# Optimization experiments

Hardware: AMD Instinct MI355X
Metric: run time of the kernel (lower is better)

## Reference

```python
import jax, jax.numpy as jnp
import numpy as np
import math

N_COARSE, N_FINE = 8192, 32768
DEC_DIM, ENC_DIM, OUT_DIM, K = 256, 128, 128, 16
LN_EPS = 1e-5


def setup_inputs() -> dict:
    key = jax.random.key(0)
    ks = jax.random.split(key, 16)
    s = lambda fan_in: 1.0 / math.sqrt(fan_in)
    return {
        "decoder_features": jax.random.normal(ks[0], (N_COARSE, DEC_DIM), jnp.float32),
        "decoder_pos": jax.random.normal(ks[1], (N_COARSE, 3), jnp.float32),
        "encoder_features": jax.random.normal(ks[2], (N_FINE, ENC_DIM), jnp.float32),
        "encoder_pos": jax.random.normal(ks[3], (N_FINE, 3), jnp.float32),
        "encoder_labels": jax.random.randint(ks[4], (N_FINE,), 0, 13, jnp.int64),
        # params (torch nn.Linear default init scale)
        "Wq": jax.random.uniform(ks[5], (DEC_DIM, ENC_DIM), jnp.float32, -s(ENC_DIM), s(ENC_DIM)),
        "bq": jnp.zeros((DEC_DIM,), jnp.float32),
        "Wk": jax.random.uniform(ks[6], (DEC_DIM, DEC_DIM), jnp.float32, -s(DEC_DIM), s(DEC_DIM)),
        "bk": jnp.zeros((DEC_DIM,), jnp.float32),
        "Wv": jax.random.uniform(ks[7], (DEC_DIM, DEC_DIM), jnp.float32, -s(DEC_DIM), s(DEC_DIM)),
        "bv": jnp.zeros((DEC_DIM,), jnp.float32),
        "W1": jax.random.uniform(ks[8], (OUT_DIM, DEC_DIM + ENC_DIM), jnp.float32, -s(DEC_DIM + ENC_DIM), s(DEC_DIM + ENC_DIM)),
        "b1": jnp.zeros((OUT_DIM,), jnp.float32),
        "W2": jax.random.uniform(ks[9], (OUT_DIM, OUT_DIM), jnp.float32, -s(OUT_DIM), s(OUT_DIM)),
        "b2": jnp.zeros((OUT_DIM,), jnp.float32),
        "ln_g": jnp.ones((OUT_DIM,), jnp.float32),
        "ln_b": jnp.zeros((OUT_DIM,), jnp.float32),
    }


def _knn_indices(encoder_pos, decoder_pos, k):
    # For each fine (encoder) point, k nearest coarse (decoder) points.
    # squared distances [N_fine, N_coarse]
    d2 = (
        jnp.sum(encoder_pos * encoder_pos, axis=1, keepdims=True)
        - 2.0 * encoder_pos @ decoder_pos.T
        + jnp.sum(decoder_pos * decoder_pos, axis=1)[None, :]
    )
    _, idx = jax.lax.top_k(-d2, k)  # [N_fine, K]
    return idx


def reference(decoder_features, decoder_pos, encoder_features, encoder_pos,
              encoder_labels, Wq, bq, Wk, bk, Wv, bv, W1, b1, W2, b2, ln_g, ln_b):
    idx = _knn_indices(encoder_pos, decoder_pos, K)            # [Nf, K]
    nbr = decoder_features[idx]                                 # [Nf, K, Dd]
    query = encoder_features @ Wq.T + bq                        # [Nf, Dd]
    keys = nbr @ Wk.T + bk                                      # [Nf, K, Dd]
    values = nbr @ Wv.T + bv                                    # [Nf, K, Dd]
    scores = jnp.einsum('nd,nkd->nk', query, keys) / math.sqrt(DEC_DIM)
    # segment softmax over edges grouped by fine target == softmax over K
    weights = jax.nn.softmax(scores, axis=-1)                   # [Nf, K]
    agg = jnp.einsum('nk,nkd->nd', weights, values)             # [Nf, Dd]
    combined = jnp.concatenate([agg, encoder_features], axis=-1)
    h = jax.nn.relu(combined @ W1.T + b1)
    up = h @ W2.T + b2                                          # [Nf, out]
    mu = jnp.mean(up, axis=-1, keepdims=True)
    var = jnp.var(up, axis=-1, keepdims=True)
    out = (up - mu) * jax.lax.rsqrt(var + LN_EPS) * ln_g + ln_b
    # dropout is identity in eval mode
    return (out, encoder_pos, encoder_labels)
```

## Files before the change

kernel.cpp:

```cpp
#include <hip/hip_runtime.h>
#include <hip/hip_bf16.h>

typedef __hip_bfloat16 bf16;
typedef unsigned short u16;

#define NC 8192
#define NF 32768
#define KNN 16
#define FMAXV 3.402823466e+38f

__device__ __forceinline__ float bfbits2f(u16 u){
  union { unsigned u; float f; } x; x.u = ((unsigned)u) << 16; return x.f;
}

__global__ __launch_bounds__(256) void k_prep(const float* __restrict__ dpos,
                                              const float* __restrict__ W1,
                                              const float* __restrict__ W2,
                                              float4* __restrict__ pos4,
                                              float4* __restrict__ W1eSa,
                                              float4* __restrict__ W1eSb,
                                              float4* __restrict__ W2Sa,
                                              float4* __restrict__ W2Sb){
  int g = blockIdx.x * 256 + threadIdx.x;
  if (g < 8192){
    float x = dpos[g * 3 + 0], y = dpos[g * 3 + 1], z = dpos[g * 3 + 2];
    float dd = __fadd_rn(__fadd_rn(__fmul_rn(x,x), __fmul_rn(y,y)), __fmul_rn(z,z));
    pos4[g] = make_float4(x, y, z, dd * 0.5f);
  } else if (g < 10240){
    int f = g - 8192; int c4 = f >> 6, jg = f & 63;
    W1eSa[f] = ((const float4*)(W1 + (size_t)(2 * jg) * 384 + 256))[c4];
  } else if (g < 12288){
    int f = g - 10240; int c4 = f >> 6, jg = f & 63;
    W1eSb[f] = ((const float4*)(W1 + (size_t)(2 * jg + 1) * 384 + 256))[c4];
  } else if (g < 14336){
    int f = g - 12288; int c4 = f >> 6, jg = f & 63;
    W2Sa[f] = ((const float4*)(W2 + (size_t)(2 * jg) * 128))[c4];
  } else if (g < 16384){
    int f = g - 14336; int c4 = f >> 6, jg = f & 63;
    W2Sb[f] = ((const float4*)(W2 + (size_t)(2 * jg + 1) * 128))[c4];
  }
}

__global__ __launch_bounds__(256) void k_wprod(const float* __restrict__ Wk,
                                               const float* __restrict__ Wv,
                                               const float* __restrict__ Wq,
                                               const float* __restrict__ W1,
                                               const float* __restrict__ bk,
                                               const float* __restrict__ bv,
                                               const float* __restrict__ bq,
                                               float* __restrict__ WkqS,
                                               float* __restrict__ WvuS,
                                               float* __restrict__ bkq,
                                               float* __restrict__ bvu,
                                               float* __restrict__ wbq,
                                               float* __restrict__ sbq){
  __shared__ float red[256];
  int b = blockIdx.x, t = threadIdx.x;
  if (b < 128){
    int c = b;
    float acc = 0.f;
    for (int j = 0; j < 256; ++j)
      acc = fmaf(Wk[(size_t)j * 256 + t], Wq[(size_t)j * 128 + c], acc);
    WkqS[(size_t)((t >> 2) * 128 + c) * 4 + (t & 3)] = acc;
    red[t] = bk[t] * Wq[(size_t)t * 128 + c];
    __syncthreads();
    for (int s = 128; s > 0; s >>= 1){ if (t < s) red[t] += red[t + s]; __syncthreads(); }
    if (t == 0) bkq[c] = red[0];
  } else if (b < 256){
    int h = b - 128;
    float acc = 0.f;
    for (int c2 = 0; c2 < 256; ++c2)
      acc = fmaf(Wv[(size_t)c2 * 256 + t], W1[(size_t)h * 384 + c2], acc);
    WvuS[(size_t)((t >> 2) * 128 + h) * 4 + (t & 3)] = acc;
    red[t] = bv[t] * W1[(size_t)h * 384 + t];
    __syncthreads();
    for (int s = 128; s > 0; s >>= 1){ if (t < s) red[t] += red[t + s]; __syncthreads(); }
    if (t == 0) bvu[h] = red[0];
  } else {
    float acc = 0.f;
    for (int j = 0; j < 256; ++j)
      acc = fmaf(Wk[(size_t)j * 256 + t], bq[j], acc);
    wbq[t] = acc;
    red[t] = bk[t] * bq[t];
    __syncthreads();
    for (int s = 128; s > 0; s >>= 1){ if (t < s) red[t] += red[t + s]; __syncthreads(); }
    if (t == 0) sbq[0] = red[0];
  }
}

__global__ __launch_bounds__(256) void k_dec(const float* __restrict__ df,
                                             const float4* __restrict__ WkqS,
                                             const float4* __restrict__ WvuS,
                                             const float* __restrict__ bkq,
                                             const float* __restrict__ bvu,
                                             const float* __restrict__ wbq,
                                             const float* __restrict__ sbq,
                                             bf16* __restrict__ Zd, bf16* __restrict__ Ud,
                                             float* __restrict__ bqK){
  __shared__ float part[16][16];
  int t = threadIdx.x;
  int g0 = blockIdx.x * 16;
  int half = __builtin_amdgcn_readfirstlane(t >> 7);
  int c = t & 127;
  const float4* W = half ? WvuS : WkqS;
  float acc[16];
  #pragma unroll
  for (int p = 0; p < 16; ++p) acc[p] = 0.f;
  for (int j4 = 0; j4 < 64; ++j4){
    float4 w = W[j4 * 128 + c];
    #pragma unroll
    for (int p = 0; p < 16; ++p){
      float4 a = ((const float4*)(df + (size_t)(g0 + p) * 256))[j4];
      acc[p] += w.x*a.x + w.y*a.y + w.z*a.z + w.w*a.w;
    }
  }
  float bias = half ? bvu[c] : bkq[c];
  bf16* dst = half ? Ud : Zd;
  #pragma unroll
  for (int p = 0; p < 16; ++p)
    dst[(size_t)(g0 + p) * 128 + c] = __float2bfloat16(acc[p] + bias);
  {
    int r = t >> 4, seg = t & 15;
    float s = 0.f;
    const float* dr = df + (size_t)(g0 + r) * 256 + seg * 16;
    const float* wq = wbq + seg * 16;
    #pragma unroll
    for (int e = 0; e < 16; ++e) s = fmaf(dr[e], wq[e], s);
    part[r][seg] = s;
  }
  __syncthreads();
  if (t < 16){
    float s = sbq[0];
    #pragma unroll
    for (int seg = 0; seg < 16; ++seg) s += part[t][seg];
    bqK[g0 + t] = s;
  }
}

__global__ __launch_bounds__(256) void k_attn(const float* __restrict__ epos,
                                              const float4* __restrict__ pos4,
                                              const float* __restrict__ ef,
                                              const bf16* __restrict__ Zd,
                                              const bf16* __restrict__ Ud,
                                              const float* __restrict__ bqK,
                                              bf16* __restrict__ hagg){
  __shared__ float smin[8 * 64];
  __shared__ float tauLDS[8];
  __shared__ int   cnt[8];
  __shared__ float lval[8][64];
  __shared__ int   lidx[8][64];

  int t = threadIdx.x, lane = t & 63, w = t >> 6;
  int n0 = blockIdx.x * 8;
  float nex[8], ney[8], nez[8];
  #pragma unroll
  for (int p = 0; p < 8; ++p){
    nex[p] = -epos[(n0 + p) * 3 + 0];
    ney[p] = -epos[(n0 + p) * 3 + 1];
    nez[p] = -epos[(n0 + p) * 3 + 2];
  }
  const float4* base = pos4 + w * 2048;

  float vmin[8] = {FMAXV,FMAXV,FMAXV,FMAXV,FMAXV,FMAXV,FMAXV,FMAXV};
  #pragma unroll 2
  for (int s = 0; s < 32; ++s){
    float4 P = base[s * 64 + lane];
    #pragma unroll
    for (int p = 0; p < 8; ++p){
      float val = fmaf(nez[p], P.z, fmaf(ney[p], P.y, fmaf(nex[p], P.x, P.w)));
      vmin[p] = fminf(vmin[p], val);
    }
  }
  #pragma unroll
  for (int k = 2; k <= 64; k <<= 1){
    #pragma unroll
    for (int j = k >> 1; j > 0; j >>= 1){
      bool keepmin = ((lane & j) == 0) == ((lane & k) == 0);
      #pragma unroll
      for (int p = 0; p < 8; ++p){
        float pv = __shfl_xor(vmin[p], j);
        vmin[p] = keepmin ? fminf(vmin[p], pv) : fmaxf(vmin[p], pv);
      }
    }
  }
  if (lane < 16){
    #pragma unroll
    for (int p = 0; p < 8; ++p) smin[p * 64 + w * 16 + lane] = vmin[p];
  }
  if (t < 8) cnt[t] = 0;
  __syncthreads();
  #pragma unroll
  for (int u = 0; u < 2; ++u){
    int p = w * 2 + u;
    float v = smin[p * 64 + lane];
    #pragma unroll
    for (int k = 2; k <= 64; k <<= 1){
      #pragma unroll
      for (int j = k >> 1; j > 0; j >>= 1){
        float pv = __shfl_xor(v, j);
        bool keepmin = ((lane & j) == 0) == ((lane & k) == 0);
        v = keepmin ? fminf(v, pv) : fmaxf(v, pv);
      }
    }
    if (lane == 16) tauLDS[p] = v;
  }
  __syncthreads();
  float tau0[8];
  #pragma unroll
  for (int p = 0; p < 8; ++p) tau0[p] = tauLDS[p];

  #pragma unroll 2
  for (int s = 0; s < 32; ++s){
    float4 P = base[s * 64 + lane];
    int cand = w * 2048 + s * 64 + lane;
    #pragma unroll
    for (int p = 0; p < 8; ++p){
      float val = fmaf(nez[p], P.z, fmaf(ney[p], P.y, fmaf(nex[p], P.x, P.w)));
      if (val <= tau0[p]){
        int slot = atomicAdd(&cnt[p], 1);
        if (slot < 64){ lval[p][slot] = val; lidx[p][slot] = cand; }
      }
    }
  }
  __syncthreads();

  for (int u = 0; u < 2; ++u){
    int p = w * 2 + u;
    int n = n0 + p;
    int c = cnt[p]; if (c > 64) c = 64;
    float v  = (lane < c) ? lval[p][lane] : FMAXV;
    int   id = (lane < c) ? lidx[p][lane] : 0x7fffffff;
    #pragma unroll
    for (int k = 2; k <= 64; k <<= 1){
      #pragma unroll
      for (int j = k >> 1; j > 0; j >>= 1){
        float pv  = __shfl_xor(v, j);
        int   pid = __shfl_xor(id, j);
        bool keepmin = ((lane & j) == 0) == ((lane & k) == 0);
        bool pless = (pv < v) || (pv == v && pid < id);
        bool take = keepmin ? pless : !pless;
        if (take){ v = pv; id = pid; }
      }
    }
    int topi = id;

    float2 eu = *(const float2*)(ef + (size_t)n * 128 + lane * 2);
    float sc = -FMAXV;
    #pragma unroll
    for (int k = 0; k < KNN; ++k){
      int ik = __shfl(topi, k);
      ushort2 zu = *(const ushort2*)((const u16*)Zd + (size_t)ik * 128 + lane * 2);
      float pr = eu.x * bfbits2f(zu.x) + eu.y * bfbits2f(zu.y);
      #pragma unroll
      for (int off = 32; off >= 1; off >>= 1) pr += __shfl_xor(pr, off);
      float bz = bqK[ik];
      if (lane == k) sc = (pr + bz) * (1.0f / 16.0f);
    }
    float mx = sc;
    #pragma unroll
    for (int off = 8; off >= 1; off >>= 1) mx = fmaxf(mx, __shfl_xor(mx, off));
    float e = (lane < KNN) ? __expf(sc - mx) : 0.f;
    float l = e;
    #pragma unroll
    for (int off = 8; off >= 1; off >>= 1) l += __shfl_xor(l, off);
    float wgt = (lane < KNN) ? (e / l) : 0.f;

    float a0 = 0.f, a1 = 0.f;
    #pragma unroll
    for (int k = 0; k < KNN; ++k){
      int ik = __shfl(topi, k);
      float wk = __shfl(wgt, k);
      ushort2 uu = *(const ushort2*)((const u16*)Ud + (size_t)ik * 128 + lane * 2);
      a0 = fmaf(wk, bfbits2f(uu.x), a0);
      a1 = fmaf(wk, bfbits2f(uu.y), a1);
    }
    bf16* hr = hagg + (size_t)n * 128 + lane * 2;
    hr[0] = __float2bfloat16(a0);
    hr[1] = __float2bfloat16(a1);
  }
}

__global__ __launch_bounds__(256) void k_mlp(const bf16* __restrict__ hagg,
                                             const float* __restrict__ ef,
                                             const float4* __restrict__ W1eSa,
                                             const float4* __restrict__ W1eSb,
                                             const float* __restrict__ b1,
                                             const float4* __restrict__ W2Sa,
                                             const float4* __restrict__ W2Sb,
                                             const float* __restrict__ b2,
                                             const float* __restrict__ lng, const float* __restrict__ lnb,
                                             const float* __restrict__ epos, const int* __restrict__ lab,
                                             float* __restrict__ out){
  __shared__ float hbuf[16 * 128];
  __shared__ float ubuf[16 * 128];
  __shared__ float stats[32];
  int t = threadIdx.x;
  int n0 = blockIdx.x * 16;
  {
    int gid = blockIdx.x * 256 + t;
    if (gid < NF){
      float* op = out + (size_t)NF * 128;
      op[gid * 3 + 0] = epos[gid * 3 + 0];
      op[gid * 3 + 1] = epos[gid * 3 + 1];
      op[gid * 3 + 2] = epos[gid * 3 + 2];
      out[(size_t)NF * 128 + (size_t)NF * 3 + gid] = (float)lab[gid];
    }
  }
  int jg = t & 63;
  int pg4 = __builtin_amdgcn_readfirstlane((t >> 6) * 4);
  int j0 = jg * 2;
  float acc[2][4];
  #pragma unroll
  for (int a = 0; a < 2; ++a)
    #pragma unroll
    for (int p = 0; p < 4; ++p) acc[a][p] = 0.f;
  for (int c4 = 0; c4 < 32; ++c4){
    float4 wa = W1eSa[c4 * 64 + jg];
    float4 wb = W1eSb[c4 * 64 + jg];
    #pragma unroll
    for (int p = 0; p < 4; ++p){
      float4 x = ((const float4*)(ef + (size_t)(n0 + pg4 + p) * 128))[c4];
      acc[0][p] += wa.x*x.x + wa.y*x.y + wa.z*x.z + wa.w*x.w;
      acc[1][p] += wb.x*x.x + wb.y*x.y + wb.z*x.z + wb.w*x.w;
    }
  }
  float b1a = b1[j0], b1b = b1[j0 + 1];
  #pragma unroll
  for (int p = 0; p < 4; ++p){
    size_t row = (size_t)(n0 + pg4 + p);
    ushort2 hgv = *(const ushort2*)((const u16*)hagg + row * 128 + j0);
    hbuf[(pg4 + p) * 128 + j0]     = fmaxf(acc[0][p] + b1a + bfbits2f(hgv.x), 0.f);
    hbuf[(pg4 + p) * 128 + j0 + 1] = fmaxf(acc[1][p] + b1b + bfbits2f(hgv.y), 0.f);
  }
  __syncthreads();
  float acc2[2][4];
  #pragma unroll
  for (int a = 0; a < 2; ++a)
    #pragma unroll
    for (int p = 0; p < 4; ++p) acc2[a][p] = 0.f;
  const float4* hb4 = (const float4*)hbuf;
  for (int c4 = 0; c4 < 32; ++c4){
    float4 wa = W2Sa[c4 * 64 + jg];
    float4 wb = W2Sb[c4 * 64 + jg];
    #pragma unroll
    for (int p = 0; p < 4; ++p){
      float4 x = hb4[(pg4 + p) * 32 + c4];
      acc2[0][p] += wa.x*x.x + wa.y*x.y + wa.z*x.z + wa.w*x.w;
      acc2[1][p] += wb.x*x.x + wb.y*x.y + wb.z*x.z + wb.w*x.w;
    }
  }
  float b2a = b2[j0], b2b = b2[j0 + 1];
  float u[2][4];
  #pragma unroll
  for (int p = 0; p < 4; ++p){
    u[0][p] = acc2[0][p] + b2a;
    u[1][p] = acc2[1][p] + b2b;
    ubuf[(pg4 + p) * 128 + j0]     = u[0][p];
    ubuf[(pg4 + p) * 128 + j0 + 1] = u[1][p];
  }
  __syncthreads();
  {
    int p = t >> 4, qi = t & 15;
    const float* ub = &ubuf[p * 128 + qi * 8];
    float s = 0.f, s2 = 0.f;
    #pragma unroll
    for (int e2i = 0; e2i < 8; ++e2i){ float v = ub[e2i]; s += v; s2 += v * v; }
    #pragma unroll
    for (int off = 1; off < 16; off <<= 1){ s += __shfl_xor(s, off); s2 += __shfl_xor(s2, off); }
    if (qi == 0){
      float mu = s * (1.f / 128.f);
      float var = s2 * (1.f / 128.f) - mu * mu;
      stats[p] = mu;
      stats[16 + p] = rsqrtf(fmaxf(var, 0.f) + 1e-5f);
    }
  }
  __syncthreads();
  float ga = lng[j0], gb = lng[j0 + 1];
  float ba = lnb[j0], bbv = lnb[j0 + 1];
  #pragma unroll
  for (int p = 0; p < 4; ++p){
    float mu = stats[pg4 + p], rs = stats[16 + pg4 + p];
    out[(size_t)(n0 + pg4 + p) * 128 + j0]     = (u[0][p] - mu) * rs * ga + ba;
    out[(size_t)(n0 + pg4 + p) * 128 + j0 + 1] = (u[1][p] - mu) * rs * gb + bbv;
  }
}

extern "C" void kernel_launch(void* const* d_in, const int* in_sizes, int n_in,
                              void* d_out, int out_size, void* d_ws, size_t ws_size,
                              hipStream_t stream){
  const float* df   = (const float*)d_in[0];
  const float* dpos = (const float*)d_in[1];
  const float* ef   = (const float*)d_in[2];
  const float* epos = (const float*)d_in[3];
  const int*   lab  = (const int*)d_in[4];
  const float* Wq = (const float*)d_in[5];
  const float* bq = (const float*)d_in[6];
  const float* Wk = (const float*)d_in[7];
  const float* bk = (const float*)d_in[8];
  const float* Wv = (const float*)d_in[9];
  const float* bv = (const float*)d_in[10];
  const float* W1 = (const float*)d_in[11];
  const float* b1 = (const float*)d_in[12];
  const float* W2 = (const float*)d_in[13];
  const float* b2 = (const float*)d_in[14];
  const float* lng = (const float*)d_in[15];
  const float* lnb = (const float*)d_in[16];
  float* out = (float*)d_out;

  char* wsb = (char*)d_ws;
  float4* pos4  = (float4*)(wsb);
  bf16*   Zd    = (bf16*)(wsb + 131072);
  bf16*   Ud    = (bf16*)(wsb + 2228224);
  float*  bqK   = (float*)(wsb + 4325376);
  bf16*   hagg  = (bf16*)(wsb + 4358144);
  float4* W1eSa = (float4*)(wsb + 12746752);
  float4* W1eSb = (float4*)(wsb + 12779520);
  float4* W2Sa  = (float4*)(wsb + 12812288);
  float4* W2Sb  = (float4*)(wsb + 12845056);
  float*  WkqS  = (float*)(wsb + 12877824);
  float*  WvuS  = (float*)(wsb + 13008896);
  float*  bkq   = (float*)(wsb + 13139968);
  float*  bvu   = (float*)(wsb + 13140480);
  float*  wbq   = (float*)(wsb + 13140992);
  float*  sbq   = (float*)(wsb + 13142016);

  k_prep  <<<64,  256, 0, stream>>>(dpos, W1, W2, pos4, W1eSa, W1eSb, W2Sa, W2Sb);
  k_wprod <<<257, 256, 0, stream>>>(Wk, Wv, Wq, W1, bk, bv, bq, WkqS, WvuS, bkq, bvu, wbq, sbq);
  k_dec   <<<NC / 16, 256, 0, stream>>>(df, (const float4*)WkqS, (const float4*)WvuS, bkq, bvu, wbq, sbq, Zd, Ud, bqK);
  k_attn  <<<NF / 8, 256, 0, stream>>>(epos, pos4, ef, Zd, Ud, bqK, hagg);
  k_mlp   <<<NF / 16, 256, 0, stream>>>(hagg, ef, W1eSa, W1eSb, b1, W2Sa, W2Sb, b2, lng, lnb, epos, lab, out);
  (void)in_sizes; (void)n_in; (void)out_size; (void)ws_size;
}
```

Measured before the change: 357.8 us.

## Fuse kNN attention with MLP/LayerNorm per wave and merge prep kernels

Merges the two setup kernels into one launch and fuses the attention and MLP kernels, so each wave owns 8 fine points and scans all coarse points itself. The kNN threshold comes from a ballot-based radix select over mapped float bits instead of bitonic merges through LDS. Reductions use DPP instead of shuffles, and the bf16 hagg round-trip through global memory is removed. In exchange each wave scans all 8192 coarse points, so per-wave work is larger with fewer cross-wave syncs. The per-point MLP is done wave-serially, and weights are re-read for every point rather than reused across a 16-point tile.

```diff
diff --git a/kernel.cpp b/kernel.cpp
--- a/kernel.cpp
+++ b/kernel.cpp
@@ -7,53 +7,49 @@
 #define NC 8192
 #define NF 32768
 #define KNN 16
+#define NPW 8
 #define FMAXV 3.402823466e+38f
 
 __device__ __forceinline__ float bfbits2f(u16 u){
   union { unsigned u; float f; } x; x.u = ((unsigned)u) << 16; return x.f;
 }
-
-__global__ __launch_bounds__(256) void k_prep(const float* __restrict__ dpos,
-                                              const float* __restrict__ W1,
-                                              const float* __restrict__ W2,
-                                              float4* __restrict__ pos4,
-                                              float4* __restrict__ W1eSa,
-                                              float4* __restrict__ W1eSb,
-                                              float4* __restrict__ W2Sa,
-                                              float4* __restrict__ W2Sb){
-  int g = blockIdx.x * 256 + threadIdx.x;
-  if (g < 8192){
-    float x = dpos[g * 3 + 0], y = dpos[g * 3 + 1], z = dpos[g * 3 + 2];
-    float dd = __fadd_rn(__fadd_rn(__fmul_rn(x,x), __fmul_rn(y,y)), __fmul_rn(z,z));
-    pos4[g] = make_float4(x, y, z, dd * 0.5f);
-  } else if (g < 10240){
-    int f = g - 8192; int c4 = f >> 6, jg = f & 63;
-    W1eSa[f] = ((const float4*)(W1 + (size_t)(2 * jg) * 384 + 256))[c4];
-  } else if (g < 12288){
-    int f = g - 10240; int c4 = f >> 6, jg = f & 63;
-    W1eSb[f] = ((const float4*)(W1 + (size_t)(2 * jg + 1) * 384 + 256))[c4];
-  } else if (g < 14336){
-    int f = g - 12288; int c4 = f >> 6, jg = f & 63;
-    W2Sa[f] = ((const float4*)(W2 + (size_t)(2 * jg) * 128))[c4];
-  } else if (g < 16384){
-    int f = g - 14336; int c4 = f >> 6, jg = f & 63;
-    W2Sb[f] = ((const float4*)(W2 + (size_t)(2 * jg + 1) * 128))[c4];
-  }
-}
-
-__global__ __launch_bounds__(256) void k_wprod(const float* __restrict__ Wk,
+__device__ __forceinline__ unsigned fmap(float f){
+  unsigned b = __float_as_uint(f);
+  return b ^ ((unsigned)((int)b >> 31) | 0x80000000u);
+}
+__device__ __forceinline__ float funmap(unsigned u){
+  unsigned b = (u & 0x80000000u) ? (u ^ 0x80000000u) : ~u;
+  return __uint_as_float(b);
+}
+__device__ __forceinline__ float wave_sum63(float x){
+  float s = x;
+  s += __int_as_float(__builtin_amdgcn_update_dpp(0, __float_as_int(s), 0x111, 0xF, 0xF, true));
+  s += __int_as_float(__builtin_amdgcn_update_dpp(0, __float_as_int(s), 0x112, 0xF, 0xF, true));
+  s += __int_as_float(__builtin_amdgcn_update_dpp(0, __float_as_int(s), 0x114, 0xF, 0xF, true));
+  s += __int_as_float(__builtin_amdgcn_update_dpp(0, __float_as_int(s), 0x118, 0xF, 0xF, true));
+  s += __int_as_float(__builtin_amdgcn_update_dpp(0, __float_as_int(s), 0x142, 0xF, 0xF, false));
+  s += __int_as_float(__builtin_amdgcn_update_dpp(0, __float_as_int(s), 0x143, 0xF, 0xF, false));
+  return s;
+}
+__device__ __forceinline__ float rdlane_f(float v, int l){
+  return __int_as_float(__builtin_amdgcn_readlane(__float_as_int(v), l));
+}
+
+__global__ __launch_bounds__(256) void k_prep2(const float* __restrict__ dpos,
+                                               const float* __restrict__ Wk,
                                                const float* __restrict__ Wv,
                                                const float* __restrict__ Wq,
                                                const float* __restrict__ W1,
+                                               const float* __restrict__ W2,
                                                const float* __restrict__ bk,
                                                const float* __restrict__ bv,
                                                const float* __restrict__ bq,
-                                               float* __restrict__ WkqS,
-                                               float* __restrict__ WvuS,
-                                               float* __restrict__ bkq,
-                                               float* __restrict__ bvu,
-                                               float* __restrict__ wbq,
-                                               float* __restrict__ sbq){
+                                               float4* __restrict__ pos4,
+                                               float4* __restrict__ W1eSa, float4* __restrict__ W1eSb,
+                                               float4* __restrict__ W2Sa,  float4* __restrict__ W2Sb,
+                                               float* __restrict__ WkqS,   float* __restrict__ WvuS,
+                                               float* __restrict__ bkq,    float* __restrict__ bvu,
+                                               float* __restrict__ wbq,    float* __restrict__ sbq){
   __shared__ float red[256];
   int b = blockIdx.x, t = threadIdx.x;
   if (b < 128){
@@ -76,7 +72,7 @@
     __syncthreads();
     for (int s = 128; s > 0; s >>= 1){ if (t < s) red[t] += red[t + s]; __syncthreads(); }
     if (t == 0) bvu[h] = red[0];
-  } else {
+  } else if (b == 256){
     float acc = 0.f;
     for (int j = 0; j < 256; ++j)
       acc = fmaf(Wk[(size_t)j * 256 + t], bq[j], acc);
@@ -85,6 +81,25 @@
     __syncthreads();
     for (int s = 128; s > 0; s >>= 1){ if (t < s) red[t] += red[t + s]; __syncthreads(); }
     if (t == 0) sbq[0] = red[0];
+  } else {
+    int g = (b - 257) * 256 + t;
+    if (g < 8192){
+      float x = dpos[g * 3 + 0], y = dpos[g * 3 + 1], z = dpos[g * 3 + 2];
+      float dd = __fadd_rn(__fadd_rn(__fmul_rn(x,x), __fmul_rn(y,y)), __fmul_rn(z,z));
+      pos4[g] = make_float4(x, y, z, dd * 0.5f);
+    } else if (g < 10240){
+      int f = g - 8192; int c4 = f >> 6, jg = f & 63;
+      W1eSa[f] = ((const float4*)(W1 + (size_t)(2 * jg) * 384 + 256))[c4];
+    } else if (g < 12288){
+      int f = g - 10240; int c4 = f >> 6, jg = f & 63;
+      W1eSb[f] = ((const float4*)(W1 + (size_t)(2 * jg + 1) * 384 + 256))[c4];
+    } else if (g < 14336){
+      int f = g - 12288; int c4 = f >> 6, jg = f & 63;
+      W2Sa[f] = ((const float4*)(W2 + (size_t)(2 * jg) * 128))[c4];
+    } else {
+      int f = g - 14336; int c4 = f >> 6, jg = f & 63;
+      W2Sb[f] = ((const float4*)(W2 + (size_t)(2 * jg + 1) * 128))[c4];
+    }
   }
 }
 
@@ -137,165 +152,28 @@
   }
 }
 
-__global__ __launch_bounds__(256) void k_attn(const float* __restrict__ epos,
-                                              const float4* __restrict__ pos4,
-                                              const float* __restrict__ ef,
-                                              const bf16* __restrict__ Zd,
-                                              const bf16* __restrict__ Ud,
-                                              const float* __restrict__ bqK,
-                                              bf16* __restrict__ hagg){
-  __shared__ float smin[8 * 64];
-  __shared__ float tauLDS[8];
-  __shared__ int   cnt[8];
-  __shared__ float lval[8][64];
-  __shared__ int   lidx[8][64];
+__global__ __launch_bounds__(256) void k_fused(const float* __restrict__ epos,
+                                               const float4* __restrict__ pos4,
+                                               const float* __restrict__ ef,
+                                               const bf16* __restrict__ Zd,
+                                               const bf16* __restrict__ Ud,
+                                               const float* __restrict__ bqK,
+                                               const float4* __restrict__ W1eSa,
+                                               const float4* __restrict__ W1eSb,
+                                               const float* __restrict__ b1,
+                                               const float4* __restrict__ W2Sa,
+                                               const float4* __restrict__ W2Sb,
+                                               const float* __restrict__ b2,
+                                               const float* __restrict__ lng,
+                                               const float* __restrict__ lnb,
+                                               const int* __restrict__ lab,
+                                               float* __restrict__ out){
+  __shared__ unsigned lu[4][NPW][64];
+  __shared__ int      li[4][NPW][64];
+  __shared__ int      cnt[4][NPW];
+  __shared__ float    hb[4][128];
 
   int t = threadIdx.x, lane = t & 63, w = t >> 6;
-  int n0 = blockIdx.x * 8;
-  float nex[8], ney[8], nez[8];
-  #pragma unroll
-  for (int p = 0; p < 8; ++p){
-    nex[p] = -epos[(n0 + p) * 3 + 0];
-    ney[p] = -epos[(n0 + p) * 3 + 1];
-    nez[p] = -epos[(n0 + p) * 3 + 2];
-  }
-  const float4* base = pos4 + w * 2048;
-
-  float vmin[8] = {FMAXV,FMAXV,FMAXV,FMAXV,FMAXV,FMAXV,FMAXV,FMAXV};
-  #pragma unroll 2
-  for (int s = 0; s < 32; ++s){
-    float4 P = base[s * 64 + lane];
-    #pragma unroll
-    for (int p = 0; p < 8; ++p){
-      float val = fmaf(nez[p], P.z, fmaf(ney[p], P.y, fmaf(nex[p], P.x, P.w)));
-      vmin[p] = fminf(vmin[p], val);
-    }
-  }
-  #pragma unroll
-  for (int k = 2; k <= 64; k <<= 1){
-    #pragma unroll
-    for (int j = k >> 1; j > 0; j >>= 1){
-      bool keepmin = ((lane & j) == 0) == ((lane & k) == 0);
-      #pragma unroll
-      for (int p = 0; p < 8; ++p){
-        float pv = __shfl_xor(vmin[p], j);
-        vmin[p] = keepmin ? fminf(vmin[p], pv) : fmaxf(vmin[p], pv);
-      }
-    }
-  }
-  if (lane < 16){
-    #pragma unroll
-    for (int p = 0; p < 8; ++p) smin[p * 64 + w * 16 + lane] = vmin[p];
-  }
-  if (t < 8) cnt[t] = 0;
-  __syncthreads();
-  #pragma unroll
-  for (int u = 0; u < 2; ++u){
-    int p = w * 2 + u;
-    float v = smin[p * 64 + lane];
-    #pragma unroll
-    for (int k = 2; k <= 64; k <<= 1){
-      #pragma unroll
-      for (int j = k >> 1; j > 0; j >>= 1){
-        float pv = __shfl_xor(v, j);
-        bool keepmin = ((lane & j) == 0) == ((lane & k) == 0);
-        v = keepmin ? fminf(v, pv) : fmaxf(v, pv);
-      }
-    }
-    if (lane == 16) tauLDS[p] = v;
-  }
-  __syncthreads();
-  float tau0[8];
-  #pragma unroll
-  for (int p = 0; p < 8; ++p) tau0[p] = tauLDS[p];
-
-  #pragma unroll 2
-  for (int s = 0; s < 32; ++s){
-    float4 P = base[s * 64 + lane];
-    int cand = w * 2048 + s * 64 + lane;
-    #pragma unroll
-    for (int p = 0; p < 8; ++p){
-      float val = fmaf(nez[p], P.z, fmaf(ney[p], P.y, fmaf(nex[p], P.x, P.w)));
-      if (val <= tau0[p]){
-        int slot = atomicAdd(&cnt[p], 1);
-        if (slot < 64){ lval[p][slot] = val; lidx[p][slot] = cand; }
-      }
-    }
-  }
-  __syncthreads();
-
-  for (int u = 0; u < 2; ++u){
-    int p = w * 2 + u;
-    int n = n0 + p;
-    int c = cnt[p]; if (c > 64) c = 64;
-    float v  = (lane < c) ? lval[p][lane] : FMAXV;
-    int   id = (lane < c) ? lidx[p][lane] : 0x7fffffff;
-    #pragma unroll
-    for (int k = 2; k <= 64; k <<= 1){
-      #pragma unroll
-      for (int j = k >> 1; j > 0; j >>= 1){
-        float pv  = __shfl_xor(v, j);
-        int   pid = __shfl_xor(id, j);
-        bool keepmin = ((lane & j) == 0) == ((lane & k) == 0);
-        bool pless = (pv < v) || (pv == v && pid < id);
-        bool take = keepmin ? pless : !pless;
-        if (take){ v = pv; id = pid; }
-      }
-    }
-    int topi = id;
-
-    float2 eu = *(const float2*)(ef + (size_t)n * 128 + lane * 2);
-    float sc = -FMAXV;
-    #pragma unroll
-    for (int k = 0; k < KNN; ++k){
-      int ik = __shfl(topi, k);
-      ushort2 zu = *(const ushort2*)((const u16*)Zd + (size_t)ik * 128 + lane * 2);
-      float pr = eu.x * bfbits2f(zu.x) + eu.y * bfbits2f(zu.y);
-      #pragma unroll
-      for (int off = 32; off >= 1; off >>= 1) pr += __shfl_xor(pr, off);
-      float bz = bqK[ik];
-      if (lane == k) sc = (pr + bz) * (1.0f / 16.0f);
-    }
-    float mx = sc;
-    #pragma unroll
-    for (int off = 8; off >= 1; off >>= 1) mx = fmaxf(mx, __shfl_xor(mx, off));
-    float e = (lane < KNN) ? __expf(sc - mx) : 0.f;
-    float l = e;
-    #pragma unroll
-    for (int off = 8; off >= 1; off >>= 1) l += __shfl_xor(l, off);
-    float wgt = (lane < KNN) ? (e / l) : 0.f;
-
-    float a0 = 0.f, a1 = 0.f;
-    #pragma unroll
-    for (int k = 0; k < KNN; ++k){
-      int ik = __shfl(topi, k);
-      float wk = __shfl(wgt, k);
-      ushort2 uu = *(const ushort2*)((const u16*)Ud + (size_t)ik * 128 + lane * 2);
-      a0 = fmaf(wk, bfbits2f(uu.x), a0);
-      a1 = fmaf(wk, bfbits2f(uu.y), a1);
-    }
-    bf16* hr = hagg + (size_t)n * 128 + lane * 2;
-    hr[0] = __float2bfloat16(a0);
-    hr[1] = __float2bfloat16(a1);
-  }
-}
-
-__global__ __launch_bounds__(256) void k_mlp(const bf16* __restrict__ hagg,
-                                             const float* __restrict__ ef,
-                                             const float4* __restrict__ W1eSa,
-                                             const float4* __restrict__ W1eSb,
-                                             const float* __restrict__ b1,
-                                             const float4* __restrict__ W2Sa,
-                                             const float4* __restrict__ W2Sb,
-                                             const float* __restrict__ b2,
-                                             const float* __restrict__ lng, const float* __restrict__ lnb,
-                                             const float* __restrict__ epos, const int* __restrict__ lab,
-                                             float* __restrict__ out){
-  __shared__ float hbuf[16 * 128];
-  __shared__ float ubuf[16 * 128];
-  __shared__ float stats[32];
-  int t = threadIdx.x;
-  int n0 = blockIdx.x * 16;
   {
     int gid = blockIdx.x * 256 + t;
     if (gid < NF){
@@ -306,82 +184,137 @@
       out[(size_t)NF * 128 + (size_t)NF * 3 + gid] = (float)lab[gid];
     }
   }
-  int jg = t & 63;
-  int pg4 = __builtin_amdgcn_readfirstlane((t >> 6) * 4);
-  int j0 = jg * 2;
-  float acc[2][4];
-  #pragma unroll
-  for (int a = 0; a < 2; ++a)
-    #pragma unroll
-    for (int p = 0; p < 4; ++p) acc[a][p] = 0.f;
-  for (int c4 = 0; c4 < 32; ++c4){
-    float4 wa = W1eSa[c4 * 64 + jg];
-    float4 wb = W1eSb[c4 * 64 + jg];
-    #pragma unroll
-    for (int p = 0; p < 4; ++p){
-      float4 x = ((const float4*)(ef + (size_t)(n0 + pg4 + p) * 128))[c4];
-      acc[0][p] += wa.x*x.x + wa.y*x.y + wa.z*x.z + wa.w*x.w;
-      acc[1][p] += wb.x*x.x + wb.y*x.y + wb.z*x.z + wb.w*x.w;
-    }
-  }
-  float b1a = b1[j0], b1b = b1[j0 + 1];
-  #pragma unroll
-  for (int p = 0; p < 4; ++p){
-    size_t row = (size_t)(n0 + pg4 + p);
-    ushort2 hgv = *(const ushort2*)((const u16*)hagg + row * 128 + j0);
-    hbuf[(pg4 + p) * 128 + j0]     = fmaxf(acc[0][p] + b1a + bfbits2f(hgv.x), 0.f);
-    hbuf[(pg4 + p) * 128 + j0 + 1] = fmaxf(acc[1][p] + b1b + bfbits2f(hgv.y), 0.f);
+  int n0 = (blockIdx.x * 4 + w) * NPW;
+  float nex[NPW], ney[NPW], nez[NPW];
+  #pragma unroll
+  for (int p = 0; p < NPW; ++p){
+    nex[p] = -epos[(n0 + p) * 3 + 0];
+    ney[p] = -epos[(n0 + p) * 3 + 1];
+    nez[p] = -epos[(n0 + p) * 3 + 2];
+  }
+  if (lane < NPW) cnt[w][lane] = 0;
+
+  float vmin[NPW];
+  #pragma unroll
+  for (int p = 0; p < NPW; ++p) vmin[p] = FMAXV;
+  #pragma unroll 4
+  for (int s = 0; s < 128; ++s){
+    float4 P = pos4[s * 64 + lane];
+    #pragma unroll
+    for (int p = 0; p < NPW; ++p){
+      float val = fmaf(nez[p], P.z, fmaf(ney[p], P.y, fmaf(nex[p], P.x, P.w)));
+      vmin[p] = fminf(vmin[p], val);
+    }
+  }
+  float tau0[NPW];
+  #pragma unroll
+  for (int p = 0; p < NPW; ++p){
+    unsigned u = fmap(vmin[p]);
+    unsigned pref = 0; int kk = 16; bool alive = true;
+    #pragma unroll
+    for (int bIt = 31; bIt >= 12; --bIt){
+      bool zero = alive && ((u & (1u << bIt)) == 0u);
+      int c = __popcll(__ballot(zero));
+      if (c >= kk){ alive = zero; }
+      else { kk -= c; alive = alive && !zero; pref |= (1u << bIt); }
+    }
+    tau0[p] = funmap(pref | 0xFFFu);
   }
   __syncthreads();
-  float acc2[2][4];
-  #pragma unroll
-  for (int a = 0; a < 2; ++a)
-    #pragma unroll
-    for (int p = 0; p < 4; ++p) acc2[a][p] = 0.f;
-  const float4* hb4 = (const float4*)hbuf;
-  for (int c4 = 0; c4 < 32; ++c4){
-    float4 wa = W2Sa[c4 * 64 + jg];
-    float4 wb = W2Sb[c4 * 64 + jg];
-    #pragma unroll
-    for (int p = 0; p < 4; ++p){
-      float4 x = hb4[(pg4 + p) * 32 + c4];
-      acc2[0][p] += wa.x*x.x + wa.y*x.y + wa.z*x.z + wa.w*x.w;
-      acc2[1][p] += wb.x*x.x + wb.y*x.y + wb.z*x.z + wb.w*x.w;
-    }
-  }
-  float b2a = b2[j0], b2b = b2[j0 + 1];
-  float u[2][4];
-  #pragma unroll
-  for (int p = 0; p < 4; ++p){
-    u[0][p] = acc2[0][p] + b2a;
-    u[1][p] = acc2[1][p] + b2b;
-    ubuf[(pg4 + p) * 128 + j0]     = u[0][p];
-    ubuf[(pg4 + p) * 128 + j0 + 1] = u[1][p];
+
+  #pragma unroll 2
+  for (int s = 0; s < 128; ++s){
+    float4 P = pos4[s * 64 + lane];
+    int cand = s * 64 + lane;
+    #pragma unroll
+    for (int p = 0; p < NPW; ++p){
+      float val = fmaf(nez[p], P.z, fmaf(ney[p], P.y, fmaf(nex[p], P.x, P.w)));
+      if (val <= tau0[p]){
+        int slot = atomicAdd(&cnt[w][p], 1);
+        if (slot < 64){ lu[w][p][slot] = fmap(val); li[w][p][slot] = cand; }
+      }
+    }
   }
   __syncthreads();
-  {
-    int p = t >> 4, qi = t & 15;
-    const float* ub = &ubuf[p * 128 + qi * 8];
-    float s = 0.f, s2 = 0.f;
-    #pragma unroll
-    for (int e2i = 0; e2i < 8; ++e2i){ float v = ub[e2i]; s += v; s2 += v * v; }
-    #pragma unroll
-    for (int off = 1; off < 16; off <<= 1){ s += __shfl_xor(s, off); s2 += __shfl_xor(s2, off); }
-    if (qi == 0){
-      float mu = s * (1.f / 128.f);
-      float var = s2 * (1.f / 128.f) - mu * mu;
-      stats[p] = mu;
-      stats[16 + p] = rsqrtf(fmaxf(var, 0.f) + 1e-5f);
-    }
-  }
-  __syncthreads();
-  float ga = lng[j0], gb = lng[j0 + 1];
-  float ba = lnb[j0], bbv = lnb[j0 + 1];
-  #pragma unroll
-  for (int p = 0; p < 4; ++p){
-    float mu = stats[pg4 + p], rs = stats[16 + pg4 + p];
-    out[(size_t)(n0 + pg4 + p) * 128 + j0]     = (u[0][p] - mu) * rs * ga + ba;
-    out[(size_t)(n0 + pg4 + p) * 128 + j0 + 1] = (u[1][p] - mu) * rs * gb + bbv;
+
+  float2 b1v = *(const float2*)(b1 + lane * 2);
+  float2 b2v = *(const float2*)(b2 + lane * 2);
+  float2 lgv = *(const float2*)(lng + lane * 2);
+  float2 lbv = *(const float2*)(lnb + lane * 2);
+
+  for (int p = 0; p < NPW; ++p){
+    int n = n0 + p;
+    int c = cnt[w][p]; if (c > 64) c = 64;
+    unsigned v = (lane < c) ? lu[w][p][lane] : 0xFFFFFFFFu;
+    int     id = (lane < c) ? li[w][p][lane] : 0x7fffffff;
+    #pragma unroll
+    for (int k = 2; k <= 64; k <<= 1){
+      #pragma unroll
+      for (int j = k >> 1; j > 0; j >>= 1){
+        unsigned pv = __shfl_xor(v, j);
+        int     pid = __shfl_xor(id, j);
+        bool keepmin = ((lane & j) == 0) == ((lane & k) == 0);
+        bool pless = (pv < v) || (pv == v && pid < id);
+        bool take = keepmin ? pless : !pless;
+        if (take){ v = pv; id = pid; }
+      }
+    }
+    float2 eu = *(const float2*)(ef + (size_t)n * 128 + lane * 2);
+    float sc[KNN];
+    int ika[KNN];
+    #pragma unroll
+    for (int k = 0; k < KNN; ++k){
+      int ik = __builtin_amdgcn_readlane(id, k);
+      ika[k] = ik;
+      ushort2 zu = *(const ushort2*)((const u16*)Zd + (size_t)ik * 128 + lane * 2);
+      float pr = eu.x * bfbits2f(zu.x) + eu.y * bfbits2f(zu.y);
+      float tot = rdlane_f(wave_sum63(pr), 63);
+      sc[k] = (tot + bqK[ik]) * (1.0f / 16.0f);
+    }
+    float mx = sc[0];
+    #pragma unroll
+    for (int k = 1; k < KNN; ++k) mx = fmaxf(mx, sc[k]);
+    float e[KNN], l = 0.f;
+    #pragma unroll
+    for (int k = 0; k < KNN; ++k){ e[k] = __expf(sc[k] - mx); l += e[k]; }
+    float invl = 1.0f / l;
+    float a0 = 0.f, a1 = 0.f;
+    #pragma unroll
+    for (int k = 0; k < KNN; ++k){
+      float wk = e[k] * invl;
+      ushort2 uu = *(const ushort2*)((const u16*)Ud + (size_t)ika[k] * 128 + lane * 2);
+      a0 = fmaf(wk, bfbits2f(uu.x), a0);
+      a1 = fmaf(wk, bfbits2f(uu.y), a1);
+    }
+    float h0 = a0 + b1v.x, h1 = a1 + b1v.y;
+    const float4* efr = (const float4*)(ef + (size_t)n * 128);
+    #pragma unroll 4
+    for (int c4 = 0; c4 < 32; ++c4){
+      float4 wa = W1eSa[c4 * 64 + lane];
+      float4 wb = W1eSb[c4 * 64 + lane];
+      float4 x = efr[c4];
+      h0 += wa.x*x.x + wa.y*x.y + wa.z*x.z + wa.w*x.w;
+      h1 += wb.x*x.x + wb.y*x.y + wb.z*x.z + wb.w*x.w;
+    }
+    h0 = fmaxf(h0, 0.f); h1 = fmaxf(h1, 0.f);
+    *(float2*)(&hb[w][lane * 2]) = make_float2(h0, h1);
+    float u0 = b2v.x, u1 = b2v.y;
+    const float4* hr = (const float4*)(&hb[w][0]);
+    #pragma unroll 4
+    for (int c4 = 0; c4 < 32; ++c4){
+      float4 wa = W2Sa[c4 * 64 + lane];
+      float4 wb = W2Sb[c4 * 64 + lane];
+      float4 x = hr[c4];
+      u0 += wa.x*x.x + wa.y*x.y + wa.z*x.z + wa.w*x.w;
+      u1 += wb.x*x.x + wb.y*x.y + wb.z*x.z + wb.w*x.w;
+    }
+    float mu = rdlane_f(wave_sum63(u0 + u1), 63) * (1.0f / 128.0f);
+    float m2 = rdlane_f(wave_sum63(u0 * u0 + u1 * u1), 63) * (1.0f / 128.0f);
+    float var = m2 - mu * mu;
+    float rs = rsqrtf(fmaxf(var, 0.f) + 1e-5f);
+    *(float2*)(out + (size_t)n * 128 + lane * 2) =
+        make_float2((u0 - mu) * rs * lgv.x + lbv.x,
+                    (u1 - mu) * rs * lgv.y + lbv.y);
   }
 }
 
@@ -412,22 +345,24 @@
   bf16*   Zd    = (bf16*)(wsb + 131072);
   bf16*   Ud    = (bf16*)(wsb + 2228224);
   float*  bqK   = (float*)(wsb + 4325376);
-  bf16*   hagg  = (bf16*)(wsb + 4358144);
-  float4* W1eSa = (float4*)(wsb + 12746752);
-  float4* W1eSb = (float4*)(wsb + 12779520);
-  float4* W2Sa  = (float4*)(wsb + 12812288);
-  float4* W2Sb  = (float4*)(wsb + 12845056);
-  float*  WkqS  = (float*)(wsb + 12877824);
-  float*  WvuS  = (float*)(wsb + 13008896);
-  float*  bkq   = (float*)(wsb + 13139968);
-  float*  bvu   = (float*)(wsb + 13140480);
-  float*  wbq   = (float*)(wsb + 13140992);
-  float*  sbq   = (float*)(wsb + 13142016);
-
-  k_prep  <<<64,  256, 0, stream>>>(dpos, W1, W2, pos4, W1eSa, W1eSb, W2Sa, W2Sb);
-  k_wprod <<<257, 256, 0, stream>>>(Wk, Wv, Wq, W1, bk, bv, bq, WkqS, WvuS, bkq, bvu, wbq, sbq);
-  k_dec   <<<NC / 16, 256, 0, stream>>>(df, (const float4*)WkqS, (const float4*)WvuS, bkq, bvu, wbq, sbq, Zd, Ud, bqK);
-  k_attn  <<<NF / 8, 256, 0, stream>>>(epos, pos4, ef, Zd, Ud, bqK, hagg);
-  k_mlp   <<<NF / 16, 256, 0, stream>>>(hagg, ef, W1eSa, W1eSb, b1, W2Sa, W2Sb, b2, lng, lnb, epos, lab, out);
+  float4* W1eSa = (float4*)(wsb + 4358144);
+  float4* W1eSb = (float4*)(wsb + 4390912);
+  float4* W2Sa  = (float4*)(wsb + 4423680);
+  float4* W2Sb  = (float4*)(wsb + 4456448);
+  float*  WkqS  = (float*)(wsb + 4489216);
+  float*  WvuS  = (float*)(wsb + 4620288);
+  float*  bkq   = (float*)(wsb + 4751360);
+  float*  bvu   = (float*)(wsb + 4751872);
+  float*  wbq   = (float*)(wsb + 4752384);
+  float*  sbq   = (float*)(wsb + 4753408);
+
+  k_prep2<<<321, 256, 0, stream>>>(dpos, Wk, Wv, Wq, W1, W2, bk, bv, bq,
+                                   pos4, W1eSa, W1eSb, W2Sa, W2Sb,
+                                   WkqS, WvuS, bkq, bvu, wbq, sbq);
+  k_dec  <<<NC / 16, 256, 0, stream>>>(df, (const float4*)WkqS, (const float4*)WvuS,
+                                       bkq, bvu, wbq, sbq, Zd, Ud, bqK);
+  k_fused<<<NF / 32, 256, 0, stream>>>(epos, pos4, ef, Zd, Ud, bqK,
+                                       W1eSa, W1eSb, b1, W2Sa, W2Sb, b2,
+                                       lng, lnb, lab, out);
   (void)in_sizes; (void)n_in; (void)out_size; (void)ws_size;
 }
```

After: 386.6 us. 8.1% more time.
